# Performance work log

Measured on AMD Instinct MI355X. Metric: run time of the kernel, lower is better.

The kernel has to match this reference:

```python
import jax, jax.numpy as jnp
import numpy as np

D_MODEL = 768
N_HEADS_CFG = 12
D_STATE = 32
D_CONV = 4
EXPAND = 2
HEADDIM = D_MODEL // N_HEADS_CFG          # 64
D_INNER = EXPAND * D_MODEL                # 1536
NHEADS = D_INNER // HEADDIM               # 24 (Mamba2 internal heads)
CONV_DIM = D_INNER + 2 * D_STATE          # 1600
D_IN_PROJ = 2 * D_INNER + 2 * D_STATE + NHEADS  # 3160
EPS = 1e-5
B_SZ, SEQ = 2, 512


def rmsnorm(x, w):
    return x * jax.lax.rsqrt(jnp.mean(x * x, axis=-1, keepdims=True) + EPS) * w


def mamba2(u, Wi, cw, cb, dtb, Alog, Dp, nw, Wo):
    """Mamba2 mixer: in_proj -> causal depthwise conv(silu) -> selective scan -> gated RMSNorm -> out_proj."""
    b, l, _ = u.shape
    zxbcdt = u @ Wi.T                                   # [b,l,d_in_proj]
    z, xBC, dt = jnp.split(zxbcdt, [D_INNER, D_INNER + CONV_DIM], axis=-1)
    # causal depthwise conv over time
    xBC = jnp.transpose(xBC, (0, 2, 1))                 # [b,c,l]
    xBC = jax.lax.conv_general_dilated(
        xBC, cw[:, None, :], window_strides=(1,),
        padding=[(D_CONV - 1, 0)], feature_group_count=CONV_DIM)
    xBC = jax.nn.silu(jnp.transpose(xBC + cb[None, :, None], (0, 2, 1)))
    x, Bm, Cm = jnp.split(xBC, [D_INNER, D_INNER + D_STATE], axis=-1)
    x = x.reshape(b, l, NHEADS, HEADDIM)                # [b,l,h,p]
    dt = jax.nn.softplus(dt + dtb)                      # [b,l,h]
    A = -jnp.exp(Alog)                                  # [h]
    a = jnp.exp(dt * A)                                 # decay [b,l,h]
    # dt * x outer B  -> [b,l,h,p,n]
    dBx = (dt[..., None, None] * x[..., None]) * Bm[:, :, None, None, :]

    def combine(e1, e2):
        a1, h1 = e1
        a2, h2 = e2
        return (a1 * a2, a2[..., None, None] * h1 + h2)

    _, h = jax.lax.associative_scan(combine, (a, dBx), axis=1)  # h: [b,l,h,p,n]
    y = jnp.einsum('blhpn,bln->blhp', h, Cm) + Dp[None, None, :, None] * x
    y = y.reshape(b, l, D_INNER)
    y = rmsnorm(y * jax.nn.silu(z), nw)                 # gated RMSNorm
    return y @ Wo.T                                     # [b,l,d_model]


def _mamba_params(key, scale=0.02):
    ks = jax.random.split(key, 6)
    return dict(
        in_w=jax.random.normal(ks[0], (D_IN_PROJ, D_MODEL), jnp.float32) * scale,
        conv_w=jax.random.normal(ks[1], (CONV_DIM, D_CONV), jnp.float32) * scale,
        conv_b=jnp.zeros((CONV_DIM,), jnp.float32),
        dt_bias=jax.random.uniform(ks[2], (NHEADS,), jnp.float32, -4.0, -1.0),
        A_log=jnp.log(jax.random.uniform(ks[3], (NHEADS,), jnp.float32, 1.0, 16.0)),
        D=jnp.ones((NHEADS,), jnp.float32),
        norm_w=jnp.ones((D_INNER,), jnp.float32),
        out_w=jax.random.normal(ks[4], (D_MODEL, D_INNER), jnp.float32) * scale,
    )


def setup_inputs() -> dict:
    key = jax.random.key(0)
    kx, kf, kb, ko = jax.random.split(key, 4)
    f = _mamba_params(kf)
    bw = _mamba_params(kb)
    return {
        'x': jax.random.normal(kx, (B_SZ, SEQ, D_MODEL), jnp.float32),
        'norm_w': jnp.ones((D_MODEL,), jnp.float32),
        'fwd_in_w': f['in_w'], 'fwd_conv_w': f['conv_w'], 'fwd_conv_b': f['conv_b'],
        'fwd_dt_bias': f['dt_bias'], 'fwd_A_log': f['A_log'], 'fwd_D': f['D'],
        'fwd_norm_w': f['norm_w'], 'fwd_out_w': f['out_w'],
        'bwd_in_w': bw['in_w'], 'bwd_conv_w': bw['conv_w'], 'bwd_conv_b': bw['conv_b'],
        'bwd_dt_bias': bw['dt_bias'], 'bwd_A_log': bw['A_log'], 'bwd_D': bw['D'],
        'bwd_norm_w': bw['norm_w'], 'bwd_out_w': bw['out_w'],
        'out_proj_w': jax.random.normal(ko, (D_MODEL, 2 * D_MODEL), jnp.float32) * 0.02,
    }


def reference(x, norm_w,
              fwd_in_w, fwd_conv_w, fwd_conv_b, fwd_dt_bias, fwd_A_log, fwd_D, fwd_norm_w, fwd_out_w,
              bwd_in_w, bwd_conv_w, bwd_conv_b, bwd_dt_bias, bwd_A_log, bwd_D, bwd_norm_w, bwd_out_w,
              out_proj_w):
    h = rmsnorm(x, norm_w)
    f_out = mamba2(h, fwd_in_w, fwd_conv_w, fwd_conv_b, fwd_dt_bias, fwd_A_log, fwd_D, fwd_norm_w, fwd_out_w)
    b_out = mamba2(h[:, ::-1], bwd_in_w, bwd_conv_w, bwd_conv_b, bwd_dt_bias, bwd_A_log, bwd_D, bwd_norm_w, bwd_out_w)[:, ::-1]
    return x + jnp.concatenate([f_out, b_out], axis=-1) @ out_proj_w.T
```

## Files before the change

kernel.cpp:

```cpp
#include <hip/hip_runtime.h>
#include <hip/hip_bf16.h>

#define DMODEL 768
#define DINNER 1536
#define DSTATE 32
#define NHEADS 24
#define HEADDIM 64
#define CONVDIM 1600
#define DINPROJ 3160
#define NPAD 3200
#define SEQ 512
#define MROWS 1024
#define CL 64
#define NCH 8

typedef __attribute__((ext_vector_type(8))) short bf16x8;
typedef __attribute__((ext_vector_type(4))) float f32x4;

__device__ __forceinline__ ushort f2bs(float v) {
  __hip_bfloat16 b = __float2bfloat16(v);
  return __builtin_bit_cast(unsigned short, b);
}
__device__ __forceinline__ float b2f(ushort u) {
  return __uint_as_float(((uint)u) << 16);
}
__device__ __forceinline__ float b2f_lo(uint u) { return __uint_as_float(u << 16); }
__device__ __forceinline__ float b2f_hi(uint u) { return __uint_as_float(u & 0xffff0000u); }

__device__ __forceinline__ void gld16(const void* g, const void* l) {
  __builtin_amdgcn_global_load_lds((const __attribute__((address_space(1))) void*)g,
                                   (__attribute__((address_space(3))) void*)l, 16, 0, 0);
}

__device__ __forceinline__ void wait_vm(int n) {
  switch (n) {
    case 0: asm volatile("s_waitcnt vmcnt(0)" ::: "memory"); break;
    case 2: asm volatile("s_waitcnt vmcnt(2)" ::: "memory"); break;
    case 3: asm volatile("s_waitcnt vmcnt(3)" ::: "memory"); break;
    case 4: asm volatile("s_waitcnt vmcnt(4)" ::: "memory"); break;
    case 6: asm volatile("s_waitcnt vmcnt(6)" ::: "memory"); break;
    default: asm volatile("s_waitcnt vmcnt(8)" ::: "memory"); break;
  }
}

__device__ __forceinline__ float block_reduce_sum(float v, float* ws4) {
#pragma unroll
  for (int o = 32; o > 0; o >>= 1) v += __shfl_xor(v, o, 64);
  int wid = threadIdx.x >> 6;
  if ((threadIdx.x & 63) == 0) ws4[wid] = v;
  __syncthreads();
  return ws4[0] + ws4[1] + ws4[2] + ws4[3];
}

__global__ __launch_bounds__(256) void prep_kernel(
    const float* __restrict__ x, const float* __restrict__ w, ushort* __restrict__ h,
    const float* __restrict__ s0, const float* __restrict__ s1,
    const float* __restrict__ s2, const float* __restrict__ s3,
    const float* __restrict__ s4, ushort* __restrict__ d) {
  if (blockIdx.x < MROWS) {
    __shared__ float ws4[4];
    int m = blockIdx.x;
    const float* xr = x + (size_t)m * DMODEL;
    float v[3];
    float ss = 0.f;
#pragma unroll
    for (int i = 0; i < 3; ++i) {
      v[i] = xr[threadIdx.x + i * 256];
      ss += v[i] * v[i];
    }
    ss = block_reduce_sum(ss, ws4);
    float sc = rsqrtf(ss / (float)DMODEL + 1e-5f);
    ushort* hr = h + (size_t)m * DMODEL;
#pragma unroll
    for (int i = 0; i < 3; ++i) {
      int c = threadIdx.x + i * 256;
      hr[c] = f2bs(v[i] * sc * w[c]);
    }
    return;
  }
  constexpr size_t NP_IN = (size_t)NPAD * DMODEL;
  constexpr size_t NE_IN = (size_t)DINPROJ * DMODEL;
  constexpr size_t NE_O = (size_t)DMODEL * DINNER;
  size_t i = (((size_t)blockIdx.x - MROWS) * 256 + threadIdx.x) * 4;
  const float* src;
  size_t off, ne;
  if (i < NP_IN) { src = s0; off = i; ne = NE_IN; }
  else if (i < 2 * NP_IN) { src = s1; off = i - NP_IN; ne = NE_IN; }
  else if (i < 2 * NP_IN + NE_O) { src = s2; off = i - 2 * NP_IN; ne = NE_O; }
  else if (i < 2 * NP_IN + 2 * NE_O) { src = s3; off = i - 2 * NP_IN - NE_O; ne = NE_O; }
  else if (i < 2 * NP_IN + 3 * NE_O) { src = s4; off = i - 2 * NP_IN - 2 * NE_O; ne = NE_O; }
  else return;
  ushort* dp = d + i;
  if (off + 3 < ne) {
    float4 v = *(const float4*)(src + off);
    dp[0] = f2bs(v.x); dp[1] = f2bs(v.y); dp[2] = f2bs(v.z); dp[3] = f2bs(v.w);
  } else {
#pragma unroll
    for (int j = 0; j < 4; ++j) dp[j] = (off + j < ne) ? f2bs(src[off + j]) : (ushort)0;
  }
}

template <int BM, int BN, bool ADD_X, bool OUT_BF16>
__global__ __launch_bounds__(256) void gemm5(
    const ushort* __restrict__ A, int lda, size_t aZ,
    const ushort* __restrict__ Bw, int ldb, size_t bZ,
    void* __restrict__ Cout, int ldc, size_t cZ,
    const float* __restrict__ X, int ldx, int K) {
  constexpr int AG = BM / 16;
  constexpr int BG = BN / 16;
  constexpr int LPT = (AG + BG) / 4;
  constexpr int MR = BM / 32;
  constexpr int NR = BN / 32;
  __shared__ ushort As[3][BM * 32];
  __shared__ ushort Bs[3][BN * 32];
  const int t = threadIdx.x, w = t >> 6, l = t & 63;
  int bx, by;
  {
    int gx = gridDim.x, gy = gridDim.y;
    int nwg = gx * gy;
    int flat = blockIdx.y * gx + blockIdx.x;
    int s = (flat & 7) * (nwg >> 3) + (flat >> 3);
    bx = s / gy; by = s % gy;
  }
  const int m0 = by * BM, n0 = bx * BN;
  const int wr = w >> 1, wc = w & 1;
  const int fr = l & 15, fq = l >> 4;
  const int sr = l >> 2, sc2 = (l & 3) * 8;
  const ushort* Ap = A + (size_t)blockIdx.z * aZ;
  const ushort* Bp = Bw + (size_t)blockIdx.z * bZ;

  auto stage = [&](int bb, int k0) {
#pragma unroll
    for (int g = w; g < AG + BG; g += 4) {
      if (g < AG)
        gld16(Ap + (size_t)(m0 + g * 16 + sr) * lda + k0 + sc2, (const char*)&As[bb][0] + g * 1024);
      else
        gld16(Bp + (size_t)(n0 + (g - AG) * 16 + sr) * ldb + k0 + sc2,
              (const char*)&Bs[bb][0] + (g - AG) * 1024);
    }
  };

  f32x4 acc[MR][NR];
#pragma unroll
  for (int m = 0; m < MR; ++m)
#pragma unroll
    for (int n = 0; n < NR; ++n) acc[m][n] = (f32x4){0.f, 0.f, 0.f, 0.f};

  const int nk = K / 32;
  stage(0, 0);
  stage(1, 32);
  stage(2, 64);
  int b = 0;
  for (int k = 0; k < nk; ++k) {
    int rem = nk - 1 - k;
    wait_vm(LPT * (rem < 2 ? rem : 2));
    __builtin_amdgcn_sched_barrier(0);
    __builtin_amdgcn_s_barrier();
    __builtin_amdgcn_sched_barrier(0);
    bf16x8 af[MR], bfr[NR];
#pragma unroll
    for (int m = 0; m < MR; ++m)
      af[m] = *(const bf16x8*)&As[b][(wr * (BM / 2) + m * 16 + fr) * 32 + fq * 8];
#pragma unroll
    for (int n = 0; n < NR; ++n)
      bfr[n] = *(const bf16x8*)&Bs[b][(wc * (BN / 2) + n * 16 + fr) * 32 + fq * 8];
#pragma unroll
    for (int m = 0; m < MR; ++m)
#pragma unroll
      for (int n = 0; n < NR; ++n)
        acc[m][n] = __builtin_amdgcn_mfma_f32_16x16x32_bf16(af[m], bfr[n], acc[m][n], 0, 0, 0);
    __builtin_amdgcn_sched_barrier(0);
    __builtin_amdgcn_s_barrier();
    if (k + 3 < nk) stage(b, (k + 3) * 32);
    b = (b == 2) ? 0 : b + 1;
  }

#pragma unroll
  for (int m = 0; m < MR; ++m) {
#pragma unroll
    for (int n = 0; n < NR; ++n) {
      int col = n0 + wc * (BN / 2) + n * 16 + fr;
#pragma unroll
      for (int j = 0; j < 4; ++j) {
        int row = m0 + wr * (BM / 2) + m * 16 + fq * 4 + j;
        float v = acc[m][n][j];
        if (ADD_X) v += X[(size_t)row * ldx + col];
        if (OUT_BF16)
          ((ushort*)Cout + (size_t)blockIdx.z * cZ)[(size_t)row * ldc + col] = f2bs(v);
        else
          ((float*)Cout + (size_t)blockIdx.z * cZ)[(size_t)row * ldc + col] = v;
      }
    }
  }
}

__global__ __launch_bounds__(256) void conv_dt_kernel(
    const ushort* __restrict__ zxb,
    const float* __restrict__ cw0, const float* __restrict__ cb0,
    const float* __restrict__ dtb0, const float* __restrict__ Al0,
    const float* __restrict__ cw1, const float* __restrict__ cb1,
    const float* __restrict__ dtb1, const float* __restrict__ Al1,
    ushort* __restrict__ xbc, float* __restrict__ dta) {
  int m = blockIdx.x;
  int dir = blockIdx.y;
  int l = m & (SEQ - 1);
  const float* cw = dir ? cw1 : cw0;
  const float* cb = dir ? cb1 : cb0;
  const ushort* zrow = zxb + (size_t)m * 6400 + dir * 3200 + DINNER;
  ushort* xo = xbc + ((size_t)dir * MROWS + m) * CONVDIM;
  for (int c = threadIdx.x; c < CONVDIM; c += 256) {
    float acc = cb[c];
    if (dir == 0) {
#pragma unroll
      for (int d = 0; d < 4; ++d) {
        if (l - d >= 0) acc = fmaf(b2f(zrow[-(ptrdiff_t)d * 6400 + c]), cw[c * 4 + 3 - d], acc);
      }
    } else {
#pragma unroll
      for (int d = 0; d < 4; ++d) {
        if (l + d < SEQ) acc = fmaf(b2f(zrow[(ptrdiff_t)d * 6400 + c]), cw[c * 4 + 3 - d], acc);
      }
    }
    xo[c] = f2bs(acc / (1.f + expf(-acc)));
  }
  if (threadIdx.x < NHEADS) {
    int hh = threadIdx.x;
    const float* dtb = dir ? dtb1 : dtb0;
    const float* Al = dir ? Al1 : Al0;
    float v = b2f(zxb[(size_t)m * 6400 + dir * 3200 + DINNER + CONVDIM + hh]) + dtb[hh];
    float dt = (v > 20.f) ? v : log1pf(expf(v));
    float A = -expf(Al[hh]);
    dta[((size_t)dir * MROWS + m) * 48 + hh] = dt;
    dta[((size_t)dir * MROWS + m) * 48 + NHEADS + hh] = expf(dt * A);
  }
}

__device__ __forceinline__ void scan_stage(
    const ushort* __restrict__ xb, int c, int dir, int h, int t,
    float xs[CL][64], float bcs[CL][64]) {
#pragma unroll
  for (int i = 0; i < 4; ++i) {
    int slot = t + i * 256;
    int s = slot >> 4, seg = (slot >> 3) & 1, o8 = slot & 7;
    int tau = c * CL + s;
    int prow = dir ? (SEQ - 1 - tau) : tau;
    const ushort* rp = xb + (size_t)prow * CONVDIM + (seg ? DINNER : h * HEADDIM) + o8 * 8;
    uint4 u = *(const uint4*)rp;
    float* dst = seg ? &bcs[s][o8 * 8] : &xs[s][o8 * 8];
    uint ua[4] = {u.x, u.y, u.z, u.w};
#pragma unroll
    for (int j = 0; j < 4; ++j) {
      dst[j * 2] = b2f_lo(ua[j]);
      dst[j * 2 + 1] = b2f_hi(ua[j]);
    }
  }
}

__global__ __launch_bounds__(256) void scan_phase1(
    const ushort* __restrict__ xbc, const float* __restrict__ dta,
    float* __restrict__ sbuf, float* __restrict__ abuf) {
  __shared__ float xs[CL][64];
  __shared__ float bcs[CL][64];
  __shared__ float das[CL][2];
  int c = blockIdx.x, bh = blockIdx.y, dir = blockIdx.z;
  int b = bh / NHEADS, h = bh % NHEADS;
  int t = threadIdx.x, p = t >> 2, q = t & 3;
  const ushort* xb = xbc + ((size_t)dir * MROWS + b * SEQ) * CONVDIM;
  scan_stage(xb, c, dir, h, t, xs, bcs);
  if (t < 128) {
    int s = t >> 1, wsel = t & 1;
    int tau = c * CL + s;
    int prow = dir ? (SEQ - 1 - tau) : tau;
    das[s][wsel] = dta[((size_t)dir * MROWS + b * SEQ + prow) * 48 + wsel * NHEADS + h];
  }
  __syncthreads();
  float hst[8];
#pragma unroll
  for (int j = 0; j < 8; ++j) hst[j] = 0.f;
  float alpha = 1.f;
#pragma unroll 8
  for (int s = 0; s < CL; ++s) {
    float xp = xs[s][p];
    float dt_s = das[s][0], a_s = das[s][1];
    float cx = dt_s * xp;
    alpha *= a_s;
    float4 B0 = *(const float4*)&bcs[s][q * 8];
    float4 B1 = *(const float4*)&bcs[s][q * 8 + 4];
    float Bv[8] = {B0.x, B0.y, B0.z, B0.w, B1.x, B1.y, B1.z, B1.w};
#pragma unroll
    for (int j = 0; j < 8; ++j) hst[j] = fmaf(a_s, hst[j], cx * Bv[j]);
  }
  float* sp = sbuf + (((size_t)(dir * 48 + bh)) * NCH + c) * 2048 + p * 32 + q * 8;
  *(float4*)sp = (float4){hst[0], hst[1], hst[2], hst[3]};
  *(float4*)(sp + 4) = (float4){hst[4], hst[5], hst[6], hst[7]};
  if (t == 0) abuf[(dir * 48 + bh) * NCH + c] = alpha;
}

__global__ __launch_bounds__(256) void scan_phase3b(
    const ushort* __restrict__ xbc, const float* __restrict__ dta,
    const float* __restrict__ sbuf, const float* __restrict__ abuf,
    const float* __restrict__ Dp0, const float* __restrict__ Dp1,
    ushort* __restrict__ yb) {
  __shared__ float xs[CL][64];
  __shared__ float bcs[CL][64];
  __shared__ float das[CL][2];
  int c = blockIdx.x, bh = blockIdx.y, dir = blockIdx.z;
  int b = bh / NHEADS, h = bh % NHEADS;
  int t = threadIdx.x, p = t >> 2, q = t & 3;
  const ushort* xb = xbc + ((size_t)dir * MROWS + b * SEQ) * CONVDIM;
  scan_stage(xb, c, dir, h, t, xs, bcs);
  if (t < 128) {
    int s = t >> 1, wsel = t & 1;
    int tau = c * CL + s;
    int prow = dir ? (SEQ - 1 - tau) : tau;
    das[s][wsel] = dta[((size_t)dir * MROWS + b * SEQ + prow) * 48 + wsel * NHEADS + h];
  }

  float hst[8];
#pragma unroll
  for (int j = 0; j < 8; ++j) hst[j] = 0.f;
  for (int cc = 0; cc < c; ++cc) {
    const float* sp = sbuf + (((size_t)(dir * 48 + bh)) * NCH + cc) * 2048 + p * 32 + q * 8;
    float4 s0 = *(const float4*)sp;
    float4 s1 = *(const float4*)(sp + 4);
    float al = abuf[(dir * 48 + bh) * NCH + cc];
    float sv[8] = {s0.x, s0.y, s0.z, s0.w, s1.x, s1.y, s1.z, s1.w};
#pragma unroll
    for (int j = 0; j < 8; ++j) hst[j] = fmaf(al, hst[j], sv[j]);
  }

  float Dv = (dir ? Dp1 : Dp0)[h];
  __syncthreads();
#pragma unroll 8
  for (int s = 0; s < CL; ++s) {
    float xp = xs[s][p];
    float dt_s = das[s][0], a_s = das[s][1];
    float cx = dt_s * xp;
    float4 B0 = *(const float4*)&bcs[s][q * 8];
    float4 B1 = *(const float4*)&bcs[s][q * 8 + 4];
    float4 C0 = *(const float4*)&bcs[s][32 + q * 8];
    float4 C1 = *(const float4*)&bcs[s][32 + q * 8 + 4];
    float Bv[8] = {B0.x, B0.y, B0.z, B0.w, B1.x, B1.y, B1.z, B1.w};
    float Cv[8] = {C0.x, C0.y, C0.z, C0.w, C1.x, C1.y, C1.z, C1.w};
    float acc = 0.f;
#pragma unroll
    for (int j = 0; j < 8; ++j) {
      hst[j] = fmaf(a_s, hst[j], cx * Bv[j]);
      acc = fmaf(hst[j], Cv[j], acc);
    }
    acc += __shfl_xor(acc, 1, 64);
    acc += __shfl_xor(acc, 2, 64);
    if (q == 0) {
      int tau = c * CL + s;
      int prow = dir ? (SEQ - 1 - tau) : tau;
      yb[((size_t)dir * MROWS + b * SEQ + prow) * DINNER + h * HEADDIM + p] =
          f2bs(fmaf(Dv, xp, acc));
    }
  }
}

__global__ __launch_bounds__(256) void gated_norm_kernel(
    const ushort* __restrict__ yb,
    const ushort* __restrict__ zxb,
    const float* __restrict__ nw0, const float* __restrict__ nw1,
    ushort* __restrict__ yn) {
  __shared__ float ws4[4];
  int m = blockIdx.x;
  int dir = blockIdx.y;
  const float* nw = dir ? nw1 : nw0;
  const uint* yrow = (const uint*)(yb + ((size_t)dir * MROWS + m) * DINNER);
  const uint* zrow = (const uint*)(zxb + (size_t)m * 6400 + dir * 3200);
  float g[6];
  float ss = 0.f;
#pragma unroll
  for (int i = 0; i < 3; ++i) {
    int c2 = threadIdx.x + i * 256;
    uint yu = yrow[c2];
    uint zu = zrow[c2];
    float y0 = b2f_lo(yu), y1 = b2f_hi(yu);
    float z0 = b2f_lo(zu), z1 = b2f_hi(zu);
    float g0 = y0 * (z0 / (1.f + expf(-z0)));
    float g1 = y1 * (z1 / (1.f + expf(-z1)));
    g[i * 2] = g0; g[i * 2 + 1] = g1;
    ss += g0 * g0 + g1 * g1;
  }
  ss = block_reduce_sum(ss, ws4);
  float sc = rsqrtf(ss / (float)DINNER + 1e-5f);
  uint* yrowo = (uint*)(yn + ((size_t)dir * MROWS + m) * DINNER);
#pragma unroll
  for (int i = 0; i < 3; ++i) {
    int c2 = threadIdx.x + i * 256;
    float2 w2 = *(const float2*)(nw + c2 * 2);
    uint lo = (uint)f2bs(g[i * 2] * sc * w2.x);
    uint hi = (uint)f2bs(g[i * 2 + 1] * sc * w2.y);
    yrowo[c2] = lo | (hi << 16);
  }
}

extern "C" void kernel_launch(void* const* d_in, const int* in_sizes, int n_in,
                              void* d_out, int out_size, void* d_ws, size_t ws_size,
                              hipStream_t stream) {
  const float* x = (const float*)d_in[0];
  const float* norm_w = (const float*)d_in[1];
  const float* in_w[2] = {(const float*)d_in[2], (const float*)d_in[10]};
  const float* conv_w[2] = {(const float*)d_in[3], (const float*)d_in[11]};
  const float* conv_b[2] = {(const float*)d_in[4], (const float*)d_in[12]};
  const float* dt_bias[2] = {(const float*)d_in[5], (const float*)d_in[13]};
  const float* A_log[2] = {(const float*)d_in[6], (const float*)d_in[14]};
  const float* Dp[2] = {(const float*)d_in[7], (const float*)d_in[15]};
  const float* nw[2] = {(const float*)d_in[8], (const float*)d_in[16]};
  const float* out_w[2] = {(const float*)d_in[9], (const float*)d_in[17]};
  const float* proj_w = (const float*)d_in[18];
  float* out = (float*)d_out;

  char* p = (char*)d_ws;
  ushort* zxb = (ushort*)p; p += (size_t)MROWS * 6400 * 2;
  ushort* xbc = (ushort*)p; p += (size_t)2 * MROWS * CONVDIM * 2;
  float* dta = (float*)p;   p += (size_t)2 * MROWS * 48 * 4;
  ushort* yb = (ushort*)p;  p += (size_t)2 * MROWS * DINNER * 2;
  float* sbuf = (float*)p;  p += (size_t)96 * NCH * 2048 * 4;
  float* abuf = (float*)p;  p += (size_t)96 * NCH * 4;
  ushort* h = (ushort*)p;   p += (size_t)MROWS * DMODEL * 2;
  ushort* yn = (ushort*)p;  p += (size_t)2 * MROWS * DINNER * 2;
  ushort* cat = (ushort*)p; p += (size_t)MROWS * DINNER * 2;
  ushort* wi = (ushort*)p;  p += (size_t)2 * NPAD * DMODEL * 2;
  ushort* wo = (ushort*)p;  p += (size_t)2 * DMODEL * DINNER * 2;
  ushort* wp = (ushort*)p;  p += (size_t)DMODEL * DINNER * 2;

  {
    size_t tot = 2 * (size_t)NPAD * DMODEL + 3 * (size_t)DMODEL * DINNER;
    int fblocks = (int)((tot / 4 + 255) / 256);
    prep_kernel<<<MROWS + fblocks, 256, 0, stream>>>(x, norm_w, h, in_w[0], in_w[1],
                                                     out_w[0], out_w[1], proj_w, wi);
  }

  {
    dim3 g(6400 / 128, MROWS / 64, 1);
    gemm5<64, 128, false, true><<<g, 256, 0, stream>>>(h, DMODEL, 0, wi, DMODEL, 0,
                                                       zxb, 6400, 0, nullptr, 0, DMODEL);
  }

  conv_dt_kernel<<<dim3(MROWS, 2), 256, 0, stream>>>(
      zxb, conv_w[0], conv_b[0], dt_bias[0], A_log[0],
      conv_w[1], conv_b[1], dt_bias[1], A_log[1], xbc, dta);

  scan_phase1<<<dim3(NCH, 48, 2), 256, 0, stream>>>(xbc, dta, sbuf, abuf);
  scan_phase3b<<<dim3(NCH, 48, 2), 256, 0, stream>>>(xbc, dta, sbuf, abuf, Dp[0], Dp[1], yb);

  gated_norm_kernel<<<dim3(MROWS, 2), 256, 0, stream>>>(yb, zxb, nw[0], nw[1], yn);

  {
    dim3 g(DMODEL / 64, MROWS / 64, 2);
    gemm5<64, 64, false, true><<<g, 256, 0, stream>>>(
        yn, DINNER, (size_t)MROWS * DINNER, wo, DINNER, (size_t)DMODEL * DINNER,
        cat, DINNER, (size_t)DMODEL, nullptr, 0, DINNER);
  }

  {
    dim3 g(DMODEL / 64, MROWS / 64, 1);
    gemm5<64, 64, true, false><<<g, 256, 0, stream>>>(cat, DINNER, 0, wp, DINNER, 0,
                                                      out, DMODEL, 0, x, DMODEL, DINNER);
  }
}
```

Measured before the change: 124.0 us.

## Replace 4-wave GEMM with single-wave 64x64 tile GEMM and deeper pipeline

```diff
diff --git a/kernel.cpp b/kernel.cpp
--- a/kernel.cpp
+++ b/kernel.cpp
@@ -35,11 +35,9 @@
 __device__ __forceinline__ void wait_vm(int n) {
   switch (n) {
     case 0: asm volatile("s_waitcnt vmcnt(0)" ::: "memory"); break;
-    case 2: asm volatile("s_waitcnt vmcnt(2)" ::: "memory"); break;
-    case 3: asm volatile("s_waitcnt vmcnt(3)" ::: "memory"); break;
-    case 4: asm volatile("s_waitcnt vmcnt(4)" ::: "memory"); break;
-    case 6: asm volatile("s_waitcnt vmcnt(6)" ::: "memory"); break;
-    default: asm volatile("s_waitcnt vmcnt(8)" ::: "memory"); break;
+    case 8: asm volatile("s_waitcnt vmcnt(8)" ::: "memory"); break;
+    case 16: asm volatile("s_waitcnt vmcnt(16)" ::: "memory"); break;
+    default: asm volatile("s_waitcnt vmcnt(24)" ::: "memory"); break;
   }
 }
 
@@ -100,20 +98,16 @@
   }
 }
 
-template <int BM, int BN, bool ADD_X, bool OUT_BF16>
-__global__ __launch_bounds__(256) void gemm5(
+template <bool ADD_X, bool OUT_BF16>
+__global__ __launch_bounds__(64) void gemm6(
     const ushort* __restrict__ A, int lda, size_t aZ,
     const ushort* __restrict__ Bw, int ldb, size_t bZ,
     void* __restrict__ Cout, int ldc, size_t cZ,
     const float* __restrict__ X, int ldx, int K) {
-  constexpr int AG = BM / 16;
-  constexpr int BG = BN / 16;
-  constexpr int LPT = (AG + BG) / 4;
-  constexpr int MR = BM / 32;
-  constexpr int NR = BN / 32;
-  __shared__ ushort As[3][BM * 32];
-  __shared__ ushort Bs[3][BN * 32];
-  const int t = threadIdx.x, w = t >> 6, l = t & 63;
+  constexpr int DEPTH = 4;
+  __shared__ ushort As[DEPTH][64 * 32];
+  __shared__ ushort Bs[DEPTH][64 * 32];
+  const int l = threadIdx.x;
   int bx, by;
   {
     int gx = gridDim.x, gy = gridDim.y;
@@ -122,8 +116,7 @@
     int s = (flat & 7) * (nwg >> 3) + (flat >> 3);
     bx = s / gy; by = s % gy;
   }
-  const int m0 = by * BM, n0 = bx * BN;
-  const int wr = w >> 1, wc = w & 1;
+  const int m0 = by * 64, n0 = bx * 64;
   const int fr = l & 15, fq = l >> 4;
   const int sr = l >> 2, sc2 = (l & 3) * 8;
   const ushort* Ap = A + (size_t)blockIdx.z * aZ;
@@ -131,58 +124,51 @@
 
   auto stage = [&](int bb, int k0) {
 #pragma unroll
-    for (int g = w; g < AG + BG; g += 4) {
-      if (g < AG)
-        gld16(Ap + (size_t)(m0 + g * 16 + sr) * lda + k0 + sc2, (const char*)&As[bb][0] + g * 1024);
-      else
-        gld16(Bp + (size_t)(n0 + (g - AG) * 16 + sr) * ldb + k0 + sc2,
-              (const char*)&Bs[bb][0] + (g - AG) * 1024);
-    }
+    for (int g = 0; g < 4; ++g)
+      gld16(Ap + (size_t)(m0 + g * 16 + sr) * lda + k0 + sc2, (const char*)&As[bb][0] + g * 1024);
+#pragma unroll
+    for (int g = 0; g < 4; ++g)
+      gld16(Bp + (size_t)(n0 + g * 16 + sr) * ldb + k0 + sc2, (const char*)&Bs[bb][0] + g * 1024);
   };
 
-  f32x4 acc[MR][NR];
-#pragma unroll
-  for (int m = 0; m < MR; ++m)
-#pragma unroll
-    for (int n = 0; n < NR; ++n) acc[m][n] = (f32x4){0.f, 0.f, 0.f, 0.f};
+  f32x4 acc[4][4];
+#pragma unroll
+  for (int m = 0; m < 4; ++m)
+#pragma unroll
+    for (int n = 0; n < 4; ++n) acc[m][n] = (f32x4){0.f, 0.f, 0.f, 0.f};
 
   const int nk = K / 32;
-  stage(0, 0);
-  stage(1, 32);
-  stage(2, 64);
+  stage(0, 0); stage(1, 32); stage(2, 64); stage(3, 96);
   int b = 0;
   for (int k = 0; k < nk; ++k) {
     int rem = nk - 1 - k;
-    wait_vm(LPT * (rem < 2 ? rem : 2));
+    wait_vm(8 * (rem < 3 ? rem : 3));
     __builtin_amdgcn_sched_barrier(0);
-    __builtin_amdgcn_s_barrier();
-    __builtin_amdgcn_sched_barrier(0);
-    bf16x8 af[MR], bfr[NR];
-#pragma unroll
-    for (int m = 0; m < MR; ++m)
-      af[m] = *(const bf16x8*)&As[b][(wr * (BM / 2) + m * 16 + fr) * 32 + fq * 8];
-#pragma unroll
-    for (int n = 0; n < NR; ++n)
-      bfr[n] = *(const bf16x8*)&Bs[b][(wc * (BN / 2) + n * 16 + fr) * 32 + fq * 8];
-#pragma unroll
-    for (int m = 0; m < MR; ++m)
-#pragma unroll
-      for (int n = 0; n < NR; ++n)
+    bf16x8 af[4], bfr[4];
+#pragma unroll
+    for (int m = 0; m < 4; ++m)
+      af[m] = *(const bf16x8*)&As[b][(m * 16 + fr) * 32 + fq * 8];
+#pragma unroll
+    for (int n = 0; n < 4; ++n)
+      bfr[n] = *(const bf16x8*)&Bs[b][(n * 16 + fr) * 32 + fq * 8];
+#pragma unroll
+    for (int m = 0; m < 4; ++m)
+#pragma unroll
+      for (int n = 0; n < 4; ++n)
         acc[m][n] = __builtin_amdgcn_mfma_f32_16x16x32_bf16(af[m], bfr[n], acc[m][n], 0, 0, 0);
     __builtin_amdgcn_sched_barrier(0);
-    __builtin_amdgcn_s_barrier();
-    if (k + 3 < nk) stage(b, (k + 3) * 32);
-    b = (b == 2) ? 0 : b + 1;
-  }
-
-#pragma unroll
-  for (int m = 0; m < MR; ++m) {
-#pragma unroll
-    for (int n = 0; n < NR; ++n) {
-      int col = n0 + wc * (BN / 2) + n * 16 + fr;
+    if (k + DEPTH < nk) stage(b, (k + DEPTH) * 32);
+    b = (b + 1) & (DEPTH - 1);
+  }
+
+#pragma unroll
+  for (int m = 0; m < 4; ++m) {
+#pragma unroll
+    for (int n = 0; n < 4; ++n) {
+      int col = n0 + n * 16 + fr;
 #pragma unroll
       for (int j = 0; j < 4; ++j) {
-        int row = m0 + wr * (BM / 2) + m * 16 + fq * 4 + j;
+        int row = m0 + m * 16 + fq * 4 + j;
         float v = acc[m][n][j];
         if (ADD_X) v += X[(size_t)row * ldx + col];
         if (OUT_BF16)
@@ -435,9 +421,9 @@
   }
 
   {
-    dim3 g(6400 / 128, MROWS / 64, 1);
-    gemm5<64, 128, false, true><<<g, 256, 0, stream>>>(h, DMODEL, 0, wi, DMODEL, 0,
-                                                       zxb, 6400, 0, nullptr, 0, DMODEL);
+    dim3 g(6400 / 64, MROWS / 64, 1);
+    gemm6<false, true><<<g, 64, 0, stream>>>(h, DMODEL, 0, wi, DMODEL, 0,
+                                             zxb, 6400, 0, nullptr, 0, DMODEL);
   }
 
   conv_dt_kernel<<<dim3(MROWS, 2), 256, 0, stream>>>(
@@ -451,14 +437,14 @@
 
   {
     dim3 g(DMODEL / 64, MROWS / 64, 2);
-    gemm5<64, 64, false, true><<<g, 256, 0, stream>>>(
+    gemm6<false, true><<<g, 64, 0, stream>>>(
         yn, DINNER, (size_t)MROWS * DINNER, wo, DINNER, (size_t)DMODEL * DINNER,
         cat, DINNER, (size_t)DMODEL, nullptr, 0, DINNER);
   }
 
   {
     dim3 g(DMODEL / 64, MROWS / 64, 1);
-    gemm5<64, 64, true, false><<<g, 256, 0, stream>>>(cat, DINNER, 0, wp, DINNER, 0,
-                                                      out, DMODEL, 0, x, DMODEL, DINNER);
-  }
-}
+    gemm6<true, false><<<g, 64, 0, stream>>>(cat, DINNER, 0, wp, DINNER, 0,
+                                             out, DMODEL, 0, x, DMODEL, DINNER);
+  }
+}
```

New measurement: 147.4 us. +18.9%, slower.

## Fuse scan phases into one kernel with flag-based inter-block chunk handoff

Applied to the files above, without the earlier changes.

```diff
diff --git a/kernel.cpp b/kernel.cpp
--- a/kernel.cpp
+++ b/kernel.cpp
@@ -56,7 +56,7 @@
     const float* __restrict__ x, const float* __restrict__ w, ushort* __restrict__ h,
     const float* __restrict__ s0, const float* __restrict__ s1,
     const float* __restrict__ s2, const float* __restrict__ s3,
-    const float* __restrict__ s4, ushort* __restrict__ d) {
+    const float* __restrict__ s4, ushort* __restrict__ d, int* __restrict__ flags) {
   if (blockIdx.x < MROWS) {
     __shared__ float ws4[4];
     int m = blockIdx.x;
@@ -77,6 +77,13 @@
       hr[c] = f2bs(v[i] * sc * w[c]);
     }
     return;
+  }
+  if (blockIdx.x == MROWS) {
+#pragma unroll
+    for (int i = 0; i < 3; ++i) {
+      int idx = threadIdx.x + i * 256;
+      if (idx < 96 * NCH) flags[idx] = 0;
+    }
   }
   constexpr size_t NP_IN = (size_t)NPAD * DMODEL;
   constexpr size_t NE_IN = (size_t)DINPROJ * DMODEL;
@@ -256,15 +263,18 @@
   }
 }
 
-__global__ __launch_bounds__(256) void scan_phase1(
+__global__ __launch_bounds__(256) void scan_fused2(
     const ushort* __restrict__ xbc, const float* __restrict__ dta,
-    float* __restrict__ sbuf, float* __restrict__ abuf) {
+    float* __restrict__ sbuf, float* __restrict__ abuf, int* __restrict__ flags,
+    const float* __restrict__ Dp0, const float* __restrict__ Dp1,
+    ushort* __restrict__ yb) {
   __shared__ float xs[CL][64];
   __shared__ float bcs[CL][64];
   __shared__ float das[CL][2];
   int c = blockIdx.x, bh = blockIdx.y, dir = blockIdx.z;
   int b = bh / NHEADS, h = bh % NHEADS;
   int t = threadIdx.x, p = t >> 2, q = t & 3;
+  int gidx = dir * 48 + bh;
   const ushort* xb = xbc + ((size_t)dir * MROWS + b * SEQ) * CONVDIM;
   scan_stage(xb, c, dir, h, t, xs, bcs);
   if (t < 128) {
@@ -274,6 +284,7 @@
     das[s][wsel] = dta[((size_t)dir * MROWS + b * SEQ + prow) * 48 + wsel * NHEADS + h];
   }
   __syncthreads();
+
   float hst[8];
 #pragma unroll
   for (int j = 0; j < 8; ++j) hst[j] = 0.f;
@@ -290,47 +301,38 @@
 #pragma unroll
     for (int j = 0; j < 8; ++j) hst[j] = fmaf(a_s, hst[j], cx * Bv[j]);
   }
-  float* sp = sbuf + (((size_t)(dir * 48 + bh)) * NCH + c) * 2048 + p * 32 + q * 8;
-  *(float4*)sp = (float4){hst[0], hst[1], hst[2], hst[3]};
-  *(float4*)(sp + 4) = (float4){hst[4], hst[5], hst[6], hst[7]};
-  if (t == 0) abuf[(dir * 48 + bh) * NCH + c] = alpha;
-}
-
-__global__ __launch_bounds__(256) void scan_phase3b(
-    const ushort* __restrict__ xbc, const float* __restrict__ dta,
-    const float* __restrict__ sbuf, const float* __restrict__ abuf,
-    const float* __restrict__ Dp0, const float* __restrict__ Dp1,
-    ushort* __restrict__ yb) {
-  __shared__ float xs[CL][64];
-  __shared__ float bcs[CL][64];
-  __shared__ float das[CL][2];
-  int c = blockIdx.x, bh = blockIdx.y, dir = blockIdx.z;
-  int b = bh / NHEADS, h = bh % NHEADS;
-  int t = threadIdx.x, p = t >> 2, q = t & 3;
-  const ushort* xb = xbc + ((size_t)dir * MROWS + b * SEQ) * CONVDIM;
-  scan_stage(xb, c, dir, h, t, xs, bcs);
-  if (t < 128) {
-    int s = t >> 1, wsel = t & 1;
-    int tau = c * CL + s;
-    int prow = dir ? (SEQ - 1 - tau) : tau;
-    das[s][wsel] = dta[((size_t)dir * MROWS + b * SEQ + prow) * 48 + wsel * NHEADS + h];
-  }
-
-  float hst[8];
+  if (c < NCH - 1) {
+    float* sp = sbuf + (((size_t)gidx) * NCH + c) * 2048 + p * 32 + q * 8;
+    *(float4*)sp = (float4){hst[0], hst[1], hst[2], hst[3]};
+    *(float4*)(sp + 4) = (float4){hst[4], hst[5], hst[6], hst[7]};
+    if (t == 0) abuf[gidx * NCH + c] = alpha;
+    __syncthreads();
+    if (t == 0)
+      __hip_atomic_store(&flags[gidx * NCH + c], 1, __ATOMIC_RELEASE,
+                         __HIP_MEMORY_SCOPE_AGENT);
+  }
+
 #pragma unroll
   for (int j = 0; j < 8; ++j) hst[j] = 0.f;
-  for (int cc = 0; cc < c; ++cc) {
-    const float* sp = sbuf + (((size_t)(dir * 48 + bh)) * NCH + cc) * 2048 + p * 32 + q * 8;
-    float4 s0 = *(const float4*)sp;
-    float4 s1 = *(const float4*)(sp + 4);
-    float al = abuf[(dir * 48 + bh) * NCH + cc];
-    float sv[8] = {s0.x, s0.y, s0.z, s0.w, s1.x, s1.y, s1.z, s1.w};
-#pragma unroll
-    for (int j = 0; j < 8; ++j) hst[j] = fmaf(al, hst[j], sv[j]);
+  if (c > 0) {
+    for (int cc = 0; cc < c; ++cc) {
+      while (__hip_atomic_load(&flags[gidx * NCH + cc], __ATOMIC_ACQUIRE,
+                               __HIP_MEMORY_SCOPE_AGENT) == 0) {
+        __builtin_amdgcn_s_sleep(8);
+      }
+    }
+    for (int cc = 0; cc < c; ++cc) {
+      const float* sp = sbuf + (((size_t)gidx) * NCH + cc) * 2048 + p * 32 + q * 8;
+      float4 s0 = *(const float4*)sp;
+      float4 s1 = *(const float4*)(sp + 4);
+      float al = abuf[gidx * NCH + cc];
+      float sv[8] = {s0.x, s0.y, s0.z, s0.w, s1.x, s1.y, s1.z, s1.w};
+#pragma unroll
+      for (int j = 0; j < 8; ++j) hst[j] = fmaf(al, hst[j], sv[j]);
+    }
   }
 
   float Dv = (dir ? Dp1 : Dp0)[h];
-  __syncthreads();
 #pragma unroll 8
   for (int s = 0; s < CL; ++s) {
     float xp = xs[s][p];
@@ -420,6 +422,7 @@
   ushort* yb = (ushort*)p;  p += (size_t)2 * MROWS * DINNER * 2;
   float* sbuf = (float*)p;  p += (size_t)96 * NCH * 2048 * 4;
   float* abuf = (float*)p;  p += (size_t)96 * NCH * 4;
+  int* flags = (int*)p;     p += (size_t)96 * NCH * 4;
   ushort* h = (ushort*)p;   p += (size_t)MROWS * DMODEL * 2;
   ushort* yn = (ushort*)p;  p += (size_t)2 * MROWS * DINNER * 2;
   ushort* cat = (ushort*)p; p += (size_t)MROWS * DINNER * 2;
@@ -431,7 +434,7 @@
     size_t tot = 2 * (size_t)NPAD * DMODEL + 3 * (size_t)DMODEL * DINNER;
     int fblocks = (int)((tot / 4 + 255) / 256);
     prep_kernel<<<MROWS + fblocks, 256, 0, stream>>>(x, norm_w, h, in_w[0], in_w[1],
-                                                     out_w[0], out_w[1], proj_w, wi);
+                                                     out_w[0], out_w[1], proj_w, wi, flags);
   }
 
   {
@@ -444,8 +447,8 @@
       zxb, conv_w[0], conv_b[0], dt_bias[0], A_log[0],
       conv_w[1], conv_b[1], dt_bias[1], A_log[1], xbc, dta);
 
-  scan_phase1<<<dim3(NCH, 48, 2), 256, 0, stream>>>(xbc, dta, sbuf, abuf);
-  scan_phase3b<<<dim3(NCH, 48, 2), 256, 0, stream>>>(xbc, dta, sbuf, abuf, Dp[0], Dp[1], yb);
+  scan_fused2<<<dim3(NCH, 48, 2), 256, 0, stream>>>(xbc, dta, sbuf, abuf, flags,
+                                                    Dp[0], Dp[1], yb);
 
   gated_norm_kernel<<<dim3(MROWS, 2), 256, 0, stream>>>(yb, zxb, nw[0], nw[1], yn);
 
```

Measured after the change: 298.7 us. 141% more time.
